# Kernel optimization log

Measured on AMD Instinct MI355X. Metric: run time of the kernel, lower is better.

## Reference

```python
import jax, jax.numpy as jnp
import numpy as np

NHEAD = 8
HEAD_DIM = 64
HIDDEN = 512
ROPE_BASE = 10000.0


def _rope_cos_sin(L, dim, dtype):
    inv_freq = 1.0 / (ROPE_BASE ** (jnp.arange(0, dim, 2, dtype=jnp.float32) / dim))
    t = jnp.arange(L, dtype=jnp.float32)
    freqs = jnp.outer(t, inv_freq)                # [L, dim/2]
    emb = jnp.concatenate([freqs, freqs], axis=-1)  # [L, dim]
    return jnp.cos(emb).astype(dtype), jnp.sin(emb).astype(dtype)


def _rotate_half(x):
    x1, x2 = jnp.split(x, 2, axis=-1)
    return jnp.concatenate([-x2, x1], axis=-1)


def setup_inputs() -> dict:
    key = jax.random.key(0)
    ks = jax.random.split(key, 5)
    B, L = 8, 1024
    scale = 0.02
    return {
        "x": jax.random.normal(ks[0], (B, L, HIDDEN), dtype=jnp.float32),
        "Wq": jax.random.normal(ks[1], (HIDDEN, HIDDEN), dtype=jnp.float32) * scale,
        "Wk": jax.random.normal(ks[2], (HIDDEN, HIDDEN), dtype=jnp.float32) * scale,
        "Wv": jax.random.normal(ks[3], (HIDDEN, HIDDEN), dtype=jnp.float32) * scale,
        "Wo": jax.random.normal(ks[4], (HIDDEN, HIDDEN), dtype=jnp.float32) * scale,
    }


def reference(x, Wq, Wk, Wv, Wo):
    B, L, _ = x.shape
    # QKV projections (nn.Linear stores weight as [out, in]; y = x @ W.T)
    def proj(W):
        y = jnp.einsum('bld,ed->ble', x, W)
        return y.reshape(B, L, NHEAD, HEAD_DIM).transpose(0, 2, 1, 3)  # [B,H,L,Dh]
    q, k, v = proj(Wq), proj(Wk), proj(Wv)

    cos, sin = _rope_cos_sin(L, HEAD_DIM, x.dtype)   # [L, Dh]
    cos = cos[None, None]                            # [1,1,L,Dh]
    sin = sin[None, None]
    q = q * cos + _rotate_half(q) * sin
    k = k * cos + _rotate_half(k) * sin

    # scaled dot-product attention (no mask, eval mode -> dropout 0)
    scores = jnp.einsum('bhqd,bhkd->bhqk', q, k) / jnp.sqrt(jnp.asarray(HEAD_DIM, x.dtype))
    attn = jax.nn.softmax(scores, axis=-1)
    out = jnp.einsum('bhqk,bhkd->bhqd', attn, v)     # [B,H,L,Dh]
    out = out.transpose(0, 2, 1, 3).reshape(B, L, HIDDEN)
    return jnp.einsum('ble,oe->blo', out, Wo)
```

## Files before the change

### kernel.cpp

```cpp
#include <hip/hip_runtime.h>
#include <math.h>


#define BB 8
#define LL 1024
#define HH 8
#define DH 64
#define HID 512

typedef __bf16 bf16x8 __attribute__((ext_vector_type(8)));
typedef float f32x4 __attribute__((ext_vector_type(4)));
typedef float f32x16 __attribute__((ext_vector_type(16)));
typedef unsigned short u16x8 __attribute__((ext_vector_type(8)));
typedef unsigned short u16x4 __attribute__((ext_vector_type(4)));
typedef unsigned u32x4 __attribute__((ext_vector_type(4)));

__device__ inline unsigned short f2bf(float f) {
    union { float f; unsigned u; } v; v.f = f;
    unsigned r = v.u + 0x7fffu + ((v.u >> 16) & 1u);
    return (unsigned short)(r >> 16);
}

__device__ inline float fexp2(float x) {
    float r;
    asm("v_exp_f32 %0, %1" : "=v"(r) : "v"(x));
    return r;
}

#define GLOAD_LDS16(g, l) __builtin_amdgcn_global_load_lds( \
    (const __attribute__((address_space(1))) unsigned int*)(g), \
    (__attribute__((address_space(3))) unsigned int*)(l), 16, 0, 0)

__device__ inline bf16x8 pack8(float e0, float e1, float e2, float e3,
                               float e4, float e5, float e6, float e7) {
    unsigned a0, a1, a2, a3;
    asm("v_cvt_pk_bf16_f32 %0, %1, %2" : "=v"(a0) : "v"(e0), "v"(e1));
    asm("v_cvt_pk_bf16_f32 %0, %1, %2" : "=v"(a1) : "v"(e2), "v"(e3));
    asm("v_cvt_pk_bf16_f32 %0, %1, %2" : "=v"(a2) : "v"(e4), "v"(e5));
    asm("v_cvt_pk_bf16_f32 %0, %1, %2" : "=v"(a3) : "v"(e6), "v"(e7));
    asm("v_permlane32_swap_b32 %0, %1" : "+v"(a0), "+v"(a2));
    asm("v_permlane32_swap_b32 %0, %1" : "+v"(a1), "+v"(a3));
    u32x4 wv; wv[0] = a0; wv[1] = a1; wv[2] = a2; wv[3] = a3;
    return *(bf16x8*)&wv;
}

#define Z16 {0.f,0.f,0.f,0.f,0.f,0.f,0.f,0.f,0.f,0.f,0.f,0.f,0.f,0.f,0.f,0.f}

__global__ __launch_bounds__(256) void convert_kernel(
    const float* __restrict__ x, const float* __restrict__ Wq,
    const float* __restrict__ Wk, const float* __restrict__ Wv,
    const float* __restrict__ Wo,
    unsigned short* __restrict__ xb, unsigned short* __restrict__ wqb,
    unsigned short* __restrict__ wkb, unsigned short* __restrict__ wvb,
    unsigned short* __restrict__ wob,
    float* __restrict__ cos_t, float* __restrict__ sin_t)
{
    int blk = blockIdx.x;
    if (blk >= 2560) {
        int idx = (blk - 2560) * 256 + threadIdx.x;
        int l = idx >> 5, j = idx & 31;
        float inv = exp2f(-(float)j * (13.287712379549449f / 32.0f));
        float th = (float)l * inv;
        cos_t[idx] = cosf(th);
        sin_t[idx] = sinf(th);
        return;
    }
    const float* s; unsigned short* d; int off;
    if (blk < 2048) { s = x; d = xb; off = blk; }
    else {
        int t = (blk - 2048) >> 7;
        off = (blk - 2048) & 127;
        s = (t == 0) ? Wq : (t == 1) ? Wk : (t == 2) ? Wv : Wo;
        d = (t == 0) ? wqb : (t == 1) ? wkb : (t == 2) ? wvb : wob;
    }
    size_t base = ((size_t)off * 256 + threadIdx.x) * 8;
    float4 a = *(const float4*)(s + base);
    float4 b = *(const float4*)(s + base + 4);
    u16x8 pk;
    pk[0] = f2bf(a.x); pk[1] = f2bf(a.y); pk[2] = f2bf(a.z); pk[3] = f2bf(a.w);
    pk[4] = f2bf(b.x); pk[5] = f2bf(b.y); pk[6] = f2bf(b.z); pk[7] = f2bf(b.w);
    *(u16x8*)(d + base) = pk;
}

__global__ __launch_bounds__(256) void qkv_gemm_kernel(
    const unsigned short* __restrict__ xb, const unsigned short* __restrict__ Wqb,
    const unsigned short* __restrict__ Wkb, const unsigned short* __restrict__ Wvb,
    const float* __restrict__ cos_t, const float* __restrict__ sin_t,
    unsigned short* __restrict__ Qb, unsigned short* __restrict__ Kb,
    unsigned short* __restrict__ Vt)
{
    __shared__ unsigned short As[128 * 64];
    __shared__ unsigned short Bs[128 * 64];

    const int mt = blockIdx.x;
    const int nt = blockIdx.y;
    const int mbase = mt * 128;
    const int mat = nt >> 2;
    const unsigned short* W = (mat == 0) ? Wqb : ((mat == 1) ? Wkb : Wvb);
    const int nW = (nt & 3) * 128;

    const int tid = threadIdx.x;
    const int w = tid >> 6, lane = tid & 63;
    const int wr = w >> 1, wc = w & 1;
    const int l15 = lane & 15, koff = (lane >> 4) * 8;

    const int srow = w * 8 + (lane >> 3);
    const int ssw = ((lane & 7) * 8) ^ (((lane >> 3) & 7) * 8);

    const int rsw = (l15 & 7) * 8;
    const int ck0 = (koff +  0) ^ rsw;
    const int ck1 = (koff + 32) ^ rsw;

    f32x4 acc[4][4];
    #pragma unroll
    for (int i = 0; i < 4; ++i)
        #pragma unroll
        for (int j = 0; j < 4; ++j) acc[i][j] = (f32x4){0.f, 0.f, 0.f, 0.f};

    for (int kc = 0; kc < 512; kc += 64) {
        __syncthreads();
        #pragma unroll
        for (int j = 0; j < 4; ++j) {
            int row = j * 32 + srow;
            GLOAD_LDS16(xb + (size_t)(mbase + row) * 512 + kc + ssw,
                        As + j * 2048 + w * 512);
            GLOAD_LDS16(W + (size_t)(nW + row) * 512 + kc + ssw,
                        Bs + j * 2048 + w * 512);
        }
        __syncthreads();

        bf16x8 af[4][2], bf[4][2];
        #pragma unroll
        for (int mi = 0; mi < 4; ++mi) {
            int r = (wr * 64 + mi * 16 + l15) * 64;
            af[mi][0] = *(const bf16x8*)&As[r + ck0];
            af[mi][1] = *(const bf16x8*)&As[r + ck1];
        }
        #pragma unroll
        for (int ni = 0; ni < 4; ++ni) {
            int r = (wc * 64 + ni * 16 + l15) * 64;
            bf[ni][0] = *(const bf16x8*)&Bs[r + ck0];
            bf[ni][1] = *(const bf16x8*)&Bs[r + ck1];
        }
        #pragma unroll
        for (int mi = 0; mi < 4; ++mi)
            #pragma unroll
            for (int ni = 0; ni < 4; ++ni) {
                acc[mi][ni] = __builtin_amdgcn_mfma_f32_16x16x32_bf16(
                    af[mi][0], bf[ni][0], acc[mi][ni], 0, 0, 0);
                acc[mi][ni] = __builtin_amdgcn_mfma_f32_16x16x32_bf16(
                    af[mi][1], bf[ni][1], acc[mi][ni], 0, 0, 0);
            }
    }

    const int h = (nt & 3) * 2 + wc;
    if (mat < 2) {
        unsigned short* D = (mat == 0) ? Qb : Kb;
        const float sc = (mat == 0) ? 0.18033688011112042f  : 1.0f;
        #pragma unroll
        for (int mi = 0; mi < 4; ++mi) {
            int m = mbase + wr * 64 + mi * 16 + (lane >> 4) * 4;
            int b = m >> 10, l0 = m & 1023;
            #pragma unroll
            for (int r = 0; r < 4; ++r) {
                int l = l0 + r;
                float c0 = cos_t[l * 32 + l15],      s0 = sin_t[l * 32 + l15];
                float c1 = cos_t[l * 32 + 16 + l15], s1 = sin_t[l * 32 + 16 + l15];
                float a0 = acc[mi][0][r], a1 = acc[mi][1][r];
                float a2 = acc[mi][2][r], a3 = acc[mi][3][r];
                float o0 = (a0 * c0 - a2 * s0) * sc;
                float o1 = (a1 * c1 - a3 * s1) * sc;
                float o2 = (a2 * c0 + a0 * s0) * sc;
                float o3 = (a3 * c1 + a1 * s1) * sc;
                size_t rowbase = ((size_t)(b * HH + h) * LL + l) * 64;
                D[rowbase +  0 + l15] = f2bf(o0);
                D[rowbase + 16 + l15] = f2bf(o1);
                D[rowbase + 32 + l15] = f2bf(o2);
                D[rowbase + 48 + l15] = f2bf(o3);
            }
        }
    } else {
        #pragma unroll
        for (int mi = 0; mi < 4; ++mi) {
            int m = mbase + wr * 64 + mi * 16 + (lane >> 4) * 4;
            int b = m >> 10, l0 = m & 1023;
            #pragma unroll
            for (int ni = 0; ni < 4; ++ni) {
                int d = ni * 16 + l15;
                u16x4 pk;
                #pragma unroll
                for (int r = 0; r < 4; ++r) pk[r] = f2bf(acc[mi][ni][r]);
                *(u16x4*)(Vt + ((size_t)(b * HH + h) * 64 + d) * LL + l0) = pk;
            }
        }
    }
}

__global__ __launch_bounds__(256) void attn_kernel(
    const unsigned short* __restrict__ Q, const unsigned short* __restrict__ K,
    const unsigned short* __restrict__ Vt, unsigned short* __restrict__ O)
{
    __shared__ unsigned short Ks[2][64 * 64];
    __shared__ unsigned short Vs[2][64 * 64];

    const int wgid = blockIdx.x;
    const int xcd = wgid & 7;
    const int j = wgid >> 3;
    const int bh = xcd * 8 + (j >> 3);
    const int qt = j & 7;
    const int b = bh >> 3, h = bh & 7;
    const int tid = threadIdx.x;
    const int w = tid >> 6;
    const int lane = tid & 63;
    const int l31 = lane & 31;
    const int hi5 = lane >> 5;

    const unsigned short* Qp = Q + (size_t)bh * LL * 64;
    const unsigned short* Kp = K + (size_t)bh * LL * 64;
    const unsigned short* Vp = Vt + (size_t)bh * 64 * LL;

    const int sr0 = w * 8 + (lane >> 3);
    const int sr1 = 32 + w * 8 + (lane >> 3);
    const int scsw = ((lane & 7) * 8) ^ (((lane >> 3) & 7) * 8);
    const int sd0 = w * 512;
    const int sd1 = 2048 + w * 512;

    const int q0 = qt * 128 + w * 32;

    bf16x8 qf0 = *(const bf16x8*)(Qp + (size_t)(q0 + l31) * 64 +  0 + hi5 * 8);
    bf16x8 qf1 = *(const bf16x8*)(Qp + (size_t)(q0 + l31) * 64 + 16 + hi5 * 8);
    bf16x8 qf2 = *(const bf16x8*)(Qp + (size_t)(q0 + l31) * 64 + 32 + hi5 * 8);
    bf16x8 qf3 = *(const bf16x8*)(Qp + (size_t)(q0 + l31) * 64 + 48 + hi5 * 8);

    const int swz = (l31 & 7) * 8;
    const int co0 = ( 0 + hi5 * 8) ^ swz;
    const int co1 = (16 + hi5 * 8) ^ swz;
    const int co2 = (32 + hi5 * 8) ^ swz;
    const int co3 = (48 + hi5 * 8) ^ swz;
    const int rA = l31 * 64;
    const int rB = (32 + l31) * 64;

    float lsum = 0.f;
    f32x16 opv0 = Z16, opv1 = Z16;

    GLOAD_LDS16(Kp + (size_t)sr0 * 64 + scsw, &Ks[0][sd0]);
    GLOAD_LDS16(Kp + (size_t)sr1 * 64 + scsw, &Ks[0][sd1]);
    GLOAD_LDS16(Vp + (size_t)sr0 * LL + scsw, &Vs[0][sd0]);
    GLOAD_LDS16(Vp + (size_t)sr1 * LL + scsw, &Vs[0][sd1]);
    __syncthreads();

    #pragma unroll 2
    for (int kt = 0; kt < 16; ++kt) {
        const int cur = kt & 1, nxt = cur ^ 1;
        const int kbase = kt * 64;

        if (kt < 15) {
            GLOAD_LDS16(Kp + (size_t)(kbase + 64 + sr0) * 64 + scsw, &Ks[nxt][sd0]);
            GLOAD_LDS16(Kp + (size_t)(kbase + 64 + sr1) * 64 + scsw, &Ks[nxt][sd1]);
            GLOAD_LDS16(Vp + (size_t)sr0 * LL + kbase + 64 + scsw, &Vs[nxt][sd0]);
            GLOAD_LDS16(Vp + (size_t)sr1 * LL + kbase + 64 + scsw, &Vs[nxt][sd1]);
            asm volatile("s_waitcnt vmcnt(4)" ::: "memory");
        } else {
            asm volatile("s_waitcnt vmcnt(0)" ::: "memory");
        }
        __builtin_amdgcn_s_barrier();

        f32x16 s0 = Z16, s1 = Z16;
        __builtin_amdgcn_s_setprio(1);
        {
            bf16x8 kA, kB;
            kA = *(const bf16x8*)&Ks[cur][rA + co0];
            kB = *(const bf16x8*)&Ks[cur][rB + co0];
            s0 = __builtin_amdgcn_mfma_f32_32x32x16_bf16(kA, qf0, s0, 0, 0, 0);
            s1 = __builtin_amdgcn_mfma_f32_32x32x16_bf16(kB, qf0, s1, 0, 0, 0);
            kA = *(const bf16x8*)&Ks[cur][rA + co1];
            kB = *(const bf16x8*)&Ks[cur][rB + co1];
            s0 = __builtin_amdgcn_mfma_f32_32x32x16_bf16(kA, qf1, s0, 0, 0, 0);
            s1 = __builtin_amdgcn_mfma_f32_32x32x16_bf16(kB, qf1, s1, 0, 0, 0);
            kA = *(const bf16x8*)&Ks[cur][rA + co2];
            kB = *(const bf16x8*)&Ks[cur][rB + co2];
            s0 = __builtin_amdgcn_mfma_f32_32x32x16_bf16(kA, qf2, s0, 0, 0, 0);
            s1 = __builtin_amdgcn_mfma_f32_32x32x16_bf16(kB, qf2, s1, 0, 0, 0);
            kA = *(const bf16x8*)&Ks[cur][rA + co3];
            kB = *(const bf16x8*)&Ks[cur][rB + co3];
            s0 = __builtin_amdgcn_mfma_f32_32x32x16_bf16(kA, qf3, s0, 0, 0, 0);
            s1 = __builtin_amdgcn_mfma_f32_32x32x16_bf16(kB, qf3, s1, 0, 0, 0);
        }
        __builtin_amdgcn_s_setprio(0);

        float e[16], f[16];
        #pragma unroll
        for (int i = 0; i < 16; ++i) e[i] = fexp2(s0[i]);
        #pragma unroll
        for (int i = 0; i < 16; ++i) f[i] = fexp2(s1[i]);
        lsum += (((e[0]+e[1])+(e[2]+e[3])) + ((e[4]+e[5])+(e[6]+e[7])))
              + (((e[8]+e[9])+(e[10]+e[11])) + ((e[12]+e[13])+(e[14]+e[15])));
        lsum += (((f[0]+f[1])+(f[2]+f[3])) + ((f[4]+f[5])+(f[6]+f[7])))
              + (((f[8]+f[9])+(f[10]+f[11])) + ((f[12]+f[13])+(f[14]+f[15])));
        bf16x8 pf0 = pack8(e[0], e[1], e[2], e[3], e[4], e[5], e[6], e[7]);
        bf16x8 pf1 = pack8(e[8], e[9], e[10], e[11], e[12], e[13], e[14], e[15]);
        bf16x8 pf2 = pack8(f[0], f[1], f[2], f[3], f[4], f[5], f[6], f[7]);
        bf16x8 pf3 = pack8(f[8], f[9], f[10], f[11], f[12], f[13], f[14], f[15]);

        __builtin_amdgcn_s_setprio(1);
        {
            bf16x8 vA, vB;
            vA = *(const bf16x8*)&Vs[cur][rA + co0];
            vB = *(const bf16x8*)&Vs[cur][rB + co0];
            opv0 = __builtin_amdgcn_mfma_f32_32x32x16_bf16(vA, pf0, opv0, 0, 0, 0);
            opv1 = __builtin_amdgcn_mfma_f32_32x32x16_bf16(vB, pf0, opv1, 0, 0, 0);
            vA = *(const bf16x8*)&Vs[cur][rA + co1];
            vB = *(const bf16x8*)&Vs[cur][rB + co1];
            opv0 = __builtin_amdgcn_mfma_f32_32x32x16_bf16(vA, pf1, opv0, 0, 0, 0);
            opv1 = __builtin_amdgcn_mfma_f32_32x32x16_bf16(vB, pf1, opv1, 0, 0, 0);
            vA = *(const bf16x8*)&Vs[cur][rA + co2];
            vB = *(const bf16x8*)&Vs[cur][rB + co2];
            opv0 = __builtin_amdgcn_mfma_f32_32x32x16_bf16(vA, pf2, opv0, 0, 0, 0);
            opv1 = __builtin_amdgcn_mfma_f32_32x32x16_bf16(vB, pf2, opv1, 0, 0, 0);
            vA = *(const bf16x8*)&Vs[cur][rA + co3];
            vB = *(const bf16x8*)&Vs[cur][rB + co3];
            opv0 = __builtin_amdgcn_mfma_f32_32x32x16_bf16(vA, pf3, opv0, 0, 0, 0);
            opv1 = __builtin_amdgcn_mfma_f32_32x32x16_bf16(vB, pf3, opv1, 0, 0, 0);
        }
        __builtin_amdgcn_s_setprio(0);

        asm volatile("" ::: "memory");
        __builtin_amdgcn_s_barrier();
    }

    lsum += __shfl_xor(lsum, 32);

    const float inv = 1.f / lsum;
    unsigned short* ob = O + (size_t)(b * LL + q0 + l31) * HID + h * 64;
    #pragma unroll
    for (int rg = 0; rg < 4; ++rg) {
        u16x4 pkA, pkB;
        #pragma unroll
        for (int rr = 0; rr < 4; ++rr) {
            pkA[rr] = f2bf(opv0[rg * 4 + rr] * inv);
            pkB[rr] = f2bf(opv1[rg * 4 + rr] * inv);
        }
        *(u16x4*)(ob + rg * 8 + hi5 * 4)      = pkA;
        *(u16x4*)(ob + 32 + rg * 8 + hi5 * 4) = pkB;
    }
}

__global__ __launch_bounds__(256) void out_gemm_kernel(
    const unsigned short* __restrict__ AOb, const unsigned short* __restrict__ Wob,
    float* __restrict__ out)
{
    __shared__ unsigned short As[128 * 32];
    __shared__ unsigned short Bs[64 * 32];

    const int mt = blockIdx.x;
    const int nt = blockIdx.y;
    const int mbase = mt * 128;
    const int nbase = nt * 64;

    const int tid = threadIdx.x;
    const int w = tid >> 6, lane = tid & 63;
    const int wr = w >> 1, wc = w & 1;
    const int l15 = lane & 15, koff = (lane >> 4) * 8;
    const int srow = (lane >> 2);
    const int scol = (lane & 3) * 8;

    f32x4 acc[4][2];
    #pragma unroll
    for (int i = 0; i < 4; ++i)
        #pragma unroll
        for (int j = 0; j < 2; ++j) acc[i][j] = (f32x4){0.f, 0.f, 0.f, 0.f};

    for (int kc = 0; kc < 512; kc += 32) {
        __syncthreads();
        #pragma unroll
        for (int j = 0; j < 2; ++j) {
            int row = w * 32 + j * 16;
            GLOAD_LDS16(AOb + (size_t)(mbase + row + srow) * 512 + kc + scol,
                        As + row * 32);
        }
        {
            int row = w * 16 + srow;
            GLOAD_LDS16(Wob + (size_t)(nbase + row) * 512 + kc + scol,
                        Bs + (w * 16) * 32);
        }
        __syncthreads();

        bf16x8 af[4], bf[2];
        #pragma unroll
        for (int mi = 0; mi < 4; ++mi)
            af[mi] = *(const bf16x8*)&As[(wr * 64 + mi * 16 + l15) * 32 + koff];
        #pragma unroll
        for (int ni = 0; ni < 2; ++ni)
            bf[ni] = *(const bf16x8*)&Bs[(wc * 32 + ni * 16 + l15) * 32 + koff];
        #pragma unroll
        for (int mi = 0; mi < 4; ++mi)
            #pragma unroll
            for (int ni = 0; ni < 2; ++ni)
                acc[mi][ni] = __builtin_amdgcn_mfma_f32_16x16x32_bf16(
                    af[mi], bf[ni], acc[mi][ni], 0, 0, 0);
    }

    #pragma unroll
    for (int mi = 0; mi < 4; ++mi) {
        int m = mbase + wr * 64 + mi * 16 + (lane >> 4) * 4;
        #pragma unroll
        for (int r = 0; r < 4; ++r) {
            size_t rowbase = (size_t)(m + r) * 512 + nbase + wc * 32;
            #pragma unroll
            for (int ni = 0; ni < 2; ++ni)
                out[rowbase + ni * 16 + l15] = acc[mi][ni][r];
        }
    }
}

extern "C" void kernel_launch(void* const* d_in, const int* in_sizes, int n_in,
                              void* d_out, int out_size, void* d_ws, size_t ws_size,
                              hipStream_t stream) {
    const float* x  = (const float*)d_in[0];
    const float* Wq = (const float*)d_in[1];
    const float* Wk = (const float*)d_in[2];
    const float* Wv = (const float*)d_in[3];
    const float* Wo = (const float*)d_in[4];
    float* out = (float*)d_out;

    const size_t tblN = (size_t)LL * 32;
    const size_t qkvN = (size_t)BB * HH * LL * 64;
    const size_t wN   = (size_t)HID * HID;

    float* cos_t = (float*)d_ws;
    float* sin_t = cos_t + tblN;
    unsigned short* Qb  = (unsigned short*)(sin_t + tblN);
    unsigned short* Kb  = Qb + qkvN;
    unsigned short* Vt  = Kb + qkvN;
    unsigned short* xb  = Vt + qkvN;
    unsigned short* Wqb = xb + qkvN;
    unsigned short* Wkb = Wqb + wN;
    unsigned short* Wvb = Wkb + wN;
    unsigned short* Wob = Wvb + wN;
    unsigned short* AOb = Wob + wN;

    hipLaunchKernelGGL(convert_kernel, dim3(2048 + 512 + 128), dim3(256), 0, stream,
                       x, Wq, Wk, Wv, Wo, xb, Wqb, Wkb, Wvb, Wob, cos_t, sin_t);
    hipLaunchKernelGGL(qkv_gemm_kernel, dim3(64, 12), dim3(256), 0, stream,
                       xb, Wqb, Wkb, Wvb, cos_t, sin_t, Qb, Kb, Vt);
    hipLaunchKernelGGL(attn_kernel, dim3(512), dim3(256), 0, stream,
                       Qb, Kb, Vt, AOb);
    hipLaunchKernelGGL(out_gemm_kernel, dim3(64, 8), dim3(256), 0, stream,
                       AOb, Wob, out);
}
```

Baseline: 73.77 us.

## Software-pipeline attention QK with PV across tiles and widen out-GEMM K tile

The attention loop now keeps four K/V LDS buffers with a prefetch distance of two tiles. Each step computes QK for tile t, then does the exp and PV for tile t-1, so score MFMAs overlap softmax work, and one barrier per iteration is removed. The output GEMM doubles its K step to 64 with an XOR-swizzled LDS layout, halving the number of sync rounds and reducing bank conflicts. The cost is more LDS per block in both kernels and more live registers, which may lower occupancy.

New measurement: 99.48 us. 34.9% more time.

```diff
diff --git a/kernel.cpp b/kernel.cpp
--- a/kernel.cpp
+++ b/kernel.cpp
@@ -200,8 +200,8 @@
     const unsigned short* __restrict__ Q, const unsigned short* __restrict__ K,
     const unsigned short* __restrict__ Vt, unsigned short* __restrict__ O)
 {
-    __shared__ unsigned short Ks[2][64 * 64];
-    __shared__ unsigned short Vs[2][64 * 64];
+    __shared__ unsigned short Ks[4][64 * 64];
+    __shared__ unsigned short Vs[4][64 * 64];
 
     const int wgid = blockIdx.x;
     const int xcd = wgid & 7;
@@ -242,91 +242,88 @@
 
     float lsum = 0.f;
     f32x16 opv0 = Z16, opv1 = Z16;
-
-    GLOAD_LDS16(Kp + (size_t)sr0 * 64 + scsw, &Ks[0][sd0]);
-    GLOAD_LDS16(Kp + (size_t)sr1 * 64 + scsw, &Ks[0][sd1]);
-    GLOAD_LDS16(Vp + (size_t)sr0 * LL + scsw, &Vs[0][sd0]);
-    GLOAD_LDS16(Vp + (size_t)sr1 * LL + scsw, &Vs[0][sd1]);
-    __syncthreads();
-
-    #pragma unroll 2
-    for (int kt = 0; kt < 16; ++kt) {
-        const int cur = kt & 1, nxt = cur ^ 1;
-        const int kbase = kt * 64;
-
-        if (kt < 15) {
-            GLOAD_LDS16(Kp + (size_t)(kbase + 64 + sr0) * 64 + scsw, &Ks[nxt][sd0]);
-            GLOAD_LDS16(Kp + (size_t)(kbase + 64 + sr1) * 64 + scsw, &Ks[nxt][sd1]);
-            GLOAD_LDS16(Vp + (size_t)sr0 * LL + kbase + 64 + scsw, &Vs[nxt][sd0]);
-            GLOAD_LDS16(Vp + (size_t)sr1 * LL + kbase + 64 + scsw, &Vs[nxt][sd1]);
+    f32x16 s0p = Z16, s1p = Z16;
+
+#define STAGE(T) do { \
+        const int _nb = (T) & 3; const int _kb = (T) * 64; \
+        GLOAD_LDS16(Kp + (size_t)(_kb + sr0) * 64 + scsw, &Ks[_nb][sd0]); \
+        GLOAD_LDS16(Kp + (size_t)(_kb + sr1) * 64 + scsw, &Ks[_nb][sd1]); \
+        GLOAD_LDS16(Vp + (size_t)sr0 * LL + _kb + scsw, &Vs[_nb][sd0]);   \
+        GLOAD_LDS16(Vp + (size_t)sr1 * LL + _kb + scsw, &Vs[_nb][sd1]);   \
+    } while (0)
+
+#define QK(T, S0, S1) do { \
+        const int _c = (T) & 3; bf16x8 _kA, _kB; \
+        _kA = *(const bf16x8*)&Ks[_c][rA + co0]; _kB = *(const bf16x8*)&Ks[_c][rB + co0]; \
+        S0 = __builtin_amdgcn_mfma_f32_32x32x16_bf16(_kA, qf0, S0, 0, 0, 0); \
+        S1 = __builtin_amdgcn_mfma_f32_32x32x16_bf16(_kB, qf0, S1, 0, 0, 0); \
+        _kA = *(const bf16x8*)&Ks[_c][rA + co1]; _kB = *(const bf16x8*)&Ks[_c][rB + co1]; \
+        S0 = __builtin_amdgcn_mfma_f32_32x32x16_bf16(_kA, qf1, S0, 0, 0, 0); \
+        S1 = __builtin_amdgcn_mfma_f32_32x32x16_bf16(_kB, qf1, S1, 0, 0, 0); \
+        _kA = *(const bf16x8*)&Ks[_c][rA + co2]; _kB = *(const bf16x8*)&Ks[_c][rB + co2]; \
+        S0 = __builtin_amdgcn_mfma_f32_32x32x16_bf16(_kA, qf2, S0, 0, 0, 0); \
+        S1 = __builtin_amdgcn_mfma_f32_32x32x16_bf16(_kB, qf2, S1, 0, 0, 0); \
+        _kA = *(const bf16x8*)&Ks[_c][rA + co3]; _kB = *(const bf16x8*)&Ks[_c][rB + co3]; \
+        S0 = __builtin_amdgcn_mfma_f32_32x32x16_bf16(_kA, qf3, S0, 0, 0, 0); \
+        S1 = __builtin_amdgcn_mfma_f32_32x32x16_bf16(_kB, qf3, S1, 0, 0, 0); \
+    } while (0)
+
+#define FINISH_PV(T) do { \
+        float e[16], f[16]; \
+        _Pragma("unroll") for (int i = 0; i < 16; ++i) e[i] = fexp2(s0p[i]); \
+        _Pragma("unroll") for (int i = 0; i < 16; ++i) f[i] = fexp2(s1p[i]); \
+        lsum += (((e[0]+e[1])+(e[2]+e[3])) + ((e[4]+e[5])+(e[6]+e[7]))) \
+              + (((e[8]+e[9])+(e[10]+e[11])) + ((e[12]+e[13])+(e[14]+e[15]))); \
+        lsum += (((f[0]+f[1])+(f[2]+f[3])) + ((f[4]+f[5])+(f[6]+f[7]))) \
+              + (((f[8]+f[9])+(f[10]+f[11])) + ((f[12]+f[13])+(f[14]+f[15]))); \
+        bf16x8 pf0 = pack8(e[0], e[1], e[2], e[3], e[4], e[5], e[6], e[7]); \
+        bf16x8 pf1 = pack8(e[8], e[9], e[10], e[11], e[12], e[13], e[14], e[15]); \
+        bf16x8 pf2 = pack8(f[0], f[1], f[2], f[3], f[4], f[5], f[6], f[7]); \
+        bf16x8 pf3 = pack8(f[8], f[9], f[10], f[11], f[12], f[13], f[14], f[15]); \
+        const int _c = (T) & 3; bf16x8 _vA, _vB; \
+        _vA = *(const bf16x8*)&Vs[_c][rA + co0]; _vB = *(const bf16x8*)&Vs[_c][rB + co0]; \
+        opv0 = __builtin_amdgcn_mfma_f32_32x32x16_bf16(_vA, pf0, opv0, 0, 0, 0); \
+        opv1 = __builtin_amdgcn_mfma_f32_32x32x16_bf16(_vB, pf0, opv1, 0, 0, 0); \
+        _vA = *(const bf16x8*)&Vs[_c][rA + co1]; _vB = *(const bf16x8*)&Vs[_c][rB + co1]; \
+        opv0 = __builtin_amdgcn_mfma_f32_32x32x16_bf16(_vA, pf1, opv0, 0, 0, 0); \
+        opv1 = __builtin_amdgcn_mfma_f32_32x32x16_bf16(_vB, pf1, opv1, 0, 0, 0); \
+        _vA = *(const bf16x8*)&Vs[_c][rA + co2]; _vB = *(const bf16x8*)&Vs[_c][rB + co2]; \
+        opv0 = __builtin_amdgcn_mfma_f32_32x32x16_bf16(_vA, pf2, opv0, 0, 0, 0); \
+        opv1 = __builtin_amdgcn_mfma_f32_32x32x16_bf16(_vB, pf2, opv1, 0, 0, 0); \
+        _vA = *(const bf16x8*)&Vs[_c][rA + co3]; _vB = *(const bf16x8*)&Vs[_c][rB + co3]; \
+        opv0 = __builtin_amdgcn_mfma_f32_32x32x16_bf16(_vA, pf3, opv0, 0, 0, 0); \
+        opv1 = __builtin_amdgcn_mfma_f32_32x32x16_bf16(_vB, pf3, opv1, 0, 0, 0); \
+    } while (0)
+
+    STAGE(0); STAGE(1); STAGE(2);
+    asm volatile("s_waitcnt vmcnt(8)" ::: "memory");
+    __builtin_amdgcn_s_barrier();
+    __builtin_amdgcn_s_setprio(1);
+    QK(0, s0p, s1p);
+    __builtin_amdgcn_s_setprio(0);
+
+    #pragma unroll
+    for (int t = 1; t < 16; ++t) {
+        if (t <= 14) {
             asm volatile("s_waitcnt vmcnt(4)" ::: "memory");
         } else {
             asm volatile("s_waitcnt vmcnt(0)" ::: "memory");
         }
         __builtin_amdgcn_s_barrier();
-
-        f32x16 s0 = Z16, s1 = Z16;
+        if (t <= 13) STAGE(t + 2);
+
+        f32x16 s0c = Z16, s1c = Z16;
         __builtin_amdgcn_s_setprio(1);
-        {
-            bf16x8 kA, kB;
-            kA = *(const bf16x8*)&Ks[cur][rA + co0];
-            kB = *(const bf16x8*)&Ks[cur][rB + co0];
-            s0 = __builtin_amdgcn_mfma_f32_32x32x16_bf16(kA, qf0, s0, 0, 0, 0);
-            s1 = __builtin_amdgcn_mfma_f32_32x32x16_bf16(kB, qf0, s1, 0, 0, 0);
-            kA = *(const bf16x8*)&Ks[cur][rA + co1];
-            kB = *(const bf16x8*)&Ks[cur][rB + co1];
-            s0 = __builtin_amdgcn_mfma_f32_32x32x16_bf16(kA, qf1, s0, 0, 0, 0);
-            s1 = __builtin_amdgcn_mfma_f32_32x32x16_bf16(kB, qf1, s1, 0, 0, 0);
-            kA = *(const bf16x8*)&Ks[cur][rA + co2];
-            kB = *(const bf16x8*)&Ks[cur][rB + co2];
-            s0 = __builtin_amdgcn_mfma_f32_32x32x16_bf16(kA, qf2, s0, 0, 0, 0);
-            s1 = __builtin_amdgcn_mfma_f32_32x32x16_bf16(kB, qf2, s1, 0, 0, 0);
-            kA = *(const bf16x8*)&Ks[cur][rA + co3];
-            kB = *(const bf16x8*)&Ks[cur][rB + co3];
-            s0 = __builtin_amdgcn_mfma_f32_32x32x16_bf16(kA, qf3, s0, 0, 0, 0);
-            s1 = __builtin_amdgcn_mfma_f32_32x32x16_bf16(kB, qf3, s1, 0, 0, 0);
-        }
+        QK(t, s0c, s1c);
         __builtin_amdgcn_s_setprio(0);
 
-        float e[16], f[16];
-        #pragma unroll
-        for (int i = 0; i < 16; ++i) e[i] = fexp2(s0[i]);
-        #pragma unroll
-        for (int i = 0; i < 16; ++i) f[i] = fexp2(s1[i]);
-        lsum += (((e[0]+e[1])+(e[2]+e[3])) + ((e[4]+e[5])+(e[6]+e[7])))
-              + (((e[8]+e[9])+(e[10]+e[11])) + ((e[12]+e[13])+(e[14]+e[15])));
-        lsum += (((f[0]+f[1])+(f[2]+f[3])) + ((f[4]+f[5])+(f[6]+f[7])))
-              + (((f[8]+f[9])+(f[10]+f[11])) + ((f[12]+f[13])+(f[14]+f[15])));
-        bf16x8 pf0 = pack8(e[0], e[1], e[2], e[3], e[4], e[5], e[6], e[7]);
-        bf16x8 pf1 = pack8(e[8], e[9], e[10], e[11], e[12], e[13], e[14], e[15]);
-        bf16x8 pf2 = pack8(f[0], f[1], f[2], f[3], f[4], f[5], f[6], f[7]);
-        bf16x8 pf3 = pack8(f[8], f[9], f[10], f[11], f[12], f[13], f[14], f[15]);
-
-        __builtin_amdgcn_s_setprio(1);
-        {
-            bf16x8 vA, vB;
-            vA = *(const bf16x8*)&Vs[cur][rA + co0];
-            vB = *(const bf16x8*)&Vs[cur][rB + co0];
-            opv0 = __builtin_amdgcn_mfma_f32_32x32x16_bf16(vA, pf0, opv0, 0, 0, 0);
-            opv1 = __builtin_amdgcn_mfma_f32_32x32x16_bf16(vB, pf0, opv1, 0, 0, 0);
-            vA = *(const bf16x8*)&Vs[cur][rA + co1];
-            vB = *(const bf16x8*)&Vs[cur][rB + co1];
-            opv0 = __builtin_amdgcn_mfma_f32_32x32x16_bf16(vA, pf1, opv0, 0, 0, 0);
-            opv1 = __builtin_amdgcn_mfma_f32_32x32x16_bf16(vB, pf1, opv1, 0, 0, 0);
-            vA = *(const bf16x8*)&Vs[cur][rA + co2];
-            vB = *(const bf16x8*)&Vs[cur][rB + co2];
-            opv0 = __builtin_amdgcn_mfma_f32_32x32x16_bf16(vA, pf2, opv0, 0, 0, 0);
-            opv1 = __builtin_amdgcn_mfma_f32_32x32x16_bf16(vB, pf2, opv1, 0, 0, 0);
-            vA = *(const bf16x8*)&Vs[cur][rA + co3];
-            vB = *(const bf16x8*)&Vs[cur][rB + co3];
-            opv0 = __builtin_amdgcn_mfma_f32_32x32x16_bf16(vA, pf3, opv0, 0, 0, 0);
-            opv1 = __builtin_amdgcn_mfma_f32_32x32x16_bf16(vB, pf3, opv1, 0, 0, 0);
-        }
-        __builtin_amdgcn_s_setprio(0);
-
+        FINISH_PV(t - 1);
+
+        s0p = s0c; s1p = s1c;
         asm volatile("" ::: "memory");
-        __builtin_amdgcn_s_barrier();
-    }
+    }
+
+    FINISH_PV(15);
 
     lsum += __shfl_xor(lsum, 32);
 
@@ -343,14 +340,17 @@
         *(u16x4*)(ob + rg * 8 + hi5 * 4)      = pkA;
         *(u16x4*)(ob + 32 + rg * 8 + hi5 * 4) = pkB;
     }
+#undef STAGE
+#undef QK
+#undef FINISH_PV
 }
 
 __global__ __launch_bounds__(256) void out_gemm_kernel(
     const unsigned short* __restrict__ AOb, const unsigned short* __restrict__ Wob,
     float* __restrict__ out)
 {
-    __shared__ unsigned short As[128 * 32];
-    __shared__ unsigned short Bs[64 * 32];
+    __shared__ unsigned short As[128 * 64];
+    __shared__ unsigned short Bs[64 * 64];
 
     const int mt = blockIdx.x;
     const int nt = blockIdx.y;
@@ -361,8 +361,12 @@
     const int w = tid >> 6, lane = tid & 63;
     const int wr = w >> 1, wc = w & 1;
     const int l15 = lane & 15, koff = (lane >> 4) * 8;
-    const int srow = (lane >> 2);
-    const int scol = (lane & 3) * 8;
+
+    const int srow = w * 8 + (lane >> 3);
+    const int ssw = ((lane & 7) * 8) ^ (((lane >> 3) & 7) * 8);
+    const int rsw = (l15 & 7) * 8;
+    const int ck0 = (koff +  0) ^ rsw;
+    const int ck1 = (koff + 32) ^ rsw;
 
     f32x4 acc[4][2];
     #pragma unroll
@@ -370,34 +374,44 @@
         #pragma unroll
         for (int j = 0; j < 2; ++j) acc[i][j] = (f32x4){0.f, 0.f, 0.f, 0.f};
 
-    for (int kc = 0; kc < 512; kc += 32) {
+    for (int kc = 0; kc < 512; kc += 64) {
         __syncthreads();
         #pragma unroll
-        for (int j = 0; j < 2; ++j) {
-            int row = w * 32 + j * 16;
-            GLOAD_LDS16(AOb + (size_t)(mbase + row + srow) * 512 + kc + scol,
-                        As + row * 32);
-        }
-        {
-            int row = w * 16 + srow;
-            GLOAD_LDS16(Wob + (size_t)(nbase + row) * 512 + kc + scol,
-                        Bs + (w * 16) * 32);
+        for (int j = 0; j < 4; ++j) {
+            int row = j * 32 + srow;
+            GLOAD_LDS16(AOb + (size_t)(mbase + row) * 512 + kc + ssw,
+                        As + j * 2048 + w * 512);
+        }
+        #pragma unroll
+        for (int c = 0; c < 2; ++c) {
+            int row = c * 32 + srow;
+            GLOAD_LDS16(Wob + (size_t)(nbase + row) * 512 + kc + ssw,
+                        Bs + c * 2048 + w * 512);
         }
         __syncthreads();
 
-        bf16x8 af[4], bf[2];
-        #pragma unroll
-        for (int mi = 0; mi < 4; ++mi)
-            af[mi] = *(const bf16x8*)&As[(wr * 64 + mi * 16 + l15) * 32 + koff];
-        #pragma unroll
-        for (int ni = 0; ni < 2; ++ni)
-            bf[ni] = *(const bf16x8*)&Bs[(wc * 32 + ni * 16 + l15) * 32 + koff];
+        bf16x8 af[4][2], bf[2][2];
+        #pragma unroll
+        for (int mi = 0; mi < 4; ++mi) {
+            int r = (wr * 64 + mi * 16 + l15) * 64;
+            af[mi][0] = *(const bf16x8*)&As[r + ck0];
+            af[mi][1] = *(const bf16x8*)&As[r + ck1];
+        }
+        #pragma unroll
+        for (int ni = 0; ni < 2; ++ni) {
+            int r = (wc * 32 + ni * 16 + l15) * 64;
+            bf[ni][0] = *(const bf16x8*)&Bs[r + ck0];
+            bf[ni][1] = *(const bf16x8*)&Bs[r + ck1];
+        }
         #pragma unroll
         for (int mi = 0; mi < 4; ++mi)
             #pragma unroll
-            for (int ni = 0; ni < 2; ++ni)
+            for (int ni = 0; ni < 2; ++ni) {
                 acc[mi][ni] = __builtin_amdgcn_mfma_f32_16x16x32_bf16(
-                    af[mi], bf[ni], acc[mi][ni], 0, 0, 0);
+                    af[mi][0], bf[ni][0], acc[mi][ni], 0, 0, 0);
+                acc[mi][ni] = __builtin_amdgcn_mfma_f32_16x16x32_bf16(
+                    af[mi][1], bf[ni][1], acc[mi][ni], 0, 0, 0);
+            }
     }
 
     #pragma unroll
```

## Double K-chunk in output GEMM and XOR-swizzle LDS layout

Applied to the files above, without the earlier changes.

The output projection GEMM now stages 64-wide K chunks per iteration instead of 32, which halves the number of barrier-synchronised load phases. The LDS tiles use an XOR swizzle on the 8-element column groups so that the fragment reads of 16 rows hit different banks. The cost is twice the shared memory per block and more registers for the fragments. The out GEMM is only a small part of the total time.

After: 72.63 us. About the same (-1.5%).

```diff
diff --git a/kernel.cpp b/kernel.cpp
--- a/kernel.cpp
+++ b/kernel.cpp
@@ -349,8 +349,8 @@
     const unsigned short* __restrict__ AOb, const unsigned short* __restrict__ Wob,
     float* __restrict__ out)
 {
-    __shared__ unsigned short As[128 * 32];
-    __shared__ unsigned short Bs[64 * 32];
+    __shared__ unsigned short As[128 * 64];
+    __shared__ unsigned short Bs[64 * 64];
 
     const int mt = blockIdx.x;
     const int nt = blockIdx.y;
@@ -361,8 +361,12 @@
     const int w = tid >> 6, lane = tid & 63;
     const int wr = w >> 1, wc = w & 1;
     const int l15 = lane & 15, koff = (lane >> 4) * 8;
-    const int srow = (lane >> 2);
-    const int scol = (lane & 3) * 8;
+
+    const int srow = w * 8 + (lane >> 3);
+    const int ssw = ((lane & 7) * 8) ^ (((lane >> 3) & 7) * 8);
+    const int rsw = (l15 & 7) * 8;
+    const int ck0 = (koff +  0) ^ rsw;
+    const int ck1 = (koff + 32) ^ rsw;
 
     f32x4 acc[4][2];
     #pragma unroll
@@ -370,34 +374,44 @@
         #pragma unroll
         for (int j = 0; j < 2; ++j) acc[i][j] = (f32x4){0.f, 0.f, 0.f, 0.f};
 
-    for (int kc = 0; kc < 512; kc += 32) {
+    for (int kc = 0; kc < 512; kc += 64) {
         __syncthreads();
         #pragma unroll
-        for (int j = 0; j < 2; ++j) {
-            int row = w * 32 + j * 16;
-            GLOAD_LDS16(AOb + (size_t)(mbase + row + srow) * 512 + kc + scol,
-                        As + row * 32);
-        }
-        {
-            int row = w * 16 + srow;
-            GLOAD_LDS16(Wob + (size_t)(nbase + row) * 512 + kc + scol,
-                        Bs + (w * 16) * 32);
+        for (int j = 0; j < 4; ++j) {
+            int row = j * 32 + srow;
+            GLOAD_LDS16(AOb + (size_t)(mbase + row) * 512 + kc + ssw,
+                        As + j * 2048 + w * 512);
+        }
+        #pragma unroll
+        for (int c = 0; c < 2; ++c) {
+            int row = c * 32 + srow;
+            GLOAD_LDS16(Wob + (size_t)(nbase + row) * 512 + kc + ssw,
+                        Bs + c * 2048 + w * 512);
         }
         __syncthreads();
 
-        bf16x8 af[4], bf[2];
-        #pragma unroll
-        for (int mi = 0; mi < 4; ++mi)
-            af[mi] = *(const bf16x8*)&As[(wr * 64 + mi * 16 + l15) * 32 + koff];
-        #pragma unroll
-        for (int ni = 0; ni < 2; ++ni)
-            bf[ni] = *(const bf16x8*)&Bs[(wc * 32 + ni * 16 + l15) * 32 + koff];
+        bf16x8 af[4][2], bf[2][2];
+        #pragma unroll
+        for (int mi = 0; mi < 4; ++mi) {
+            int r = (wr * 64 + mi * 16 + l15) * 64;
+            af[mi][0] = *(const bf16x8*)&As[r + ck0];
+            af[mi][1] = *(const bf16x8*)&As[r + ck1];
+        }
+        #pragma unroll
+        for (int ni = 0; ni < 2; ++ni) {
+            int r = (wc * 32 + ni * 16 + l15) * 64;
+            bf[ni][0] = *(const bf16x8*)&Bs[r + ck0];
+            bf[ni][1] = *(const bf16x8*)&Bs[r + ck1];
+        }
         #pragma unroll
         for (int mi = 0; mi < 4; ++mi)
             #pragma unroll
-            for (int ni = 0; ni < 2; ++ni)
+            for (int ni = 0; ni < 2; ++ni) {
                 acc[mi][ni] = __builtin_amdgcn_mfma_f32_16x16x32_bf16(
-                    af[mi], bf[ni], acc[mi][ni], 0, 0, 0);
+                    af[mi][0], bf[ni][0], acc[mi][ni], 0, 0, 0);
+                acc[mi][ni] = __builtin_amdgcn_mfma_f32_16x16x32_bf16(
+                    af[mi][1], bf[ni][1], acc[mi][ni], 0, 0, 0);
+            }
     }
 
     #pragma unroll
```
